# Kernel tuning notes

Measured on AMD Instinct MI355X. Metric: run time of the kernel, lower is better.

## Reference

```python
import jax, jax.numpy as jnp
import numpy as np

D_MODEL = 1024
NUM_HEADS = 16
D_K = D_MODEL // NUM_HEADS
THETA = 10000.0
MAX_SEQ_LEN = 2048
BATCH = 2
SEQ = 2048


def setup_inputs() -> dict:
    key = jax.random.key(0)
    ks = jax.random.split(key, 5)
    std = np.sqrt(2.0 / (D_MODEL + D_MODEL)).astype(np.float32)
    x = jax.random.normal(ks[0], (BATCH, SEQ, D_MODEL), dtype=jnp.float32)
    Wq = jax.random.normal(ks[1], (D_MODEL, D_MODEL), dtype=jnp.float32) * std
    Wk = jax.random.normal(ks[2], (D_MODEL, D_MODEL), dtype=jnp.float32) * std
    Wv = jax.random.normal(ks[3], (D_MODEL, D_MODEL), dtype=jnp.float32) * std
    Wo = jax.random.normal(ks[4], (D_MODEL, D_MODEL), dtype=jnp.float32) * std
    token_positions = jnp.arange(SEQ, dtype=jnp.int32)
    return {"x": x, "token_positions": token_positions,
            "Wq": Wq, "Wk": Wk, "Wv": Wv, "Wo": Wo}


def _rope_tables(positions):
    # freqs: [d_k/2]; angles: [seq, d_k/2]
    freqs = 1.0 / (THETA ** (jnp.arange(0, D_K, 2, dtype=jnp.float32) / D_K))
    angles = positions.astype(jnp.float32)[:, None] * freqs[None, :]
    return jnp.cos(angles), jnp.sin(angles)


def _apply_rope(t, cos, sin):
    # t: [b, h, s, d_k]; cos/sin: [s, d_k/2]; interleaved pair rotation
    x1 = t[..., 0::2]
    x2 = t[..., 1::2]
    r1 = x1 * cos - x2 * sin
    r2 = x1 * sin + x2 * cos
    return jnp.stack([r1, r2], axis=-1).reshape(t.shape)


def reference(x, token_positions, Wq, Wk, Wv, Wo):
    b, s, _ = x.shape
    # projections: y = x W^T
    q = jnp.einsum('bsi,oi->bso', x, Wq)
    k = jnp.einsum('bsi,oi->bso', x, Wk)
    v = jnp.einsum('bsi,oi->bso', x, Wv)
    # split heads: [b, h, s, d]
    q = q.reshape(b, s, NUM_HEADS, D_K).transpose(0, 2, 1, 3)
    k = k.reshape(b, s, NUM_HEADS, D_K).transpose(0, 2, 1, 3)
    v = v.reshape(b, s, NUM_HEADS, D_K).transpose(0, 2, 1, 3)
    cos, sin = _rope_tables(token_positions)
    q = _apply_rope(q, cos, sin)
    k = _apply_rope(k, cos, sin)
    scale = jnp.asarray(D_K, jnp.float32) ** 0.5
    scores = jnp.einsum('bhqd,bhkd->bhqk', q, k) / scale
    causal = jnp.tril(jnp.ones((s, s), dtype=bool))
    scores = jnp.where(causal, scores, -jnp.inf)
    attn = jax.nn.softmax(scores.astype(jnp.float32), axis=-1).astype(scores.dtype)
    out = jnp.einsum('bhqk,bhkd->bhqd', attn, v)
    out = out.transpose(0, 2, 1, 3).reshape(b, s, D_MODEL)
    return jnp.einsum('bsi,oi->bso', out, Wo)
```

## Files before the change

### kernel.cpp

```cpp
#include <hip/hip_runtime.h>
#include <stdint.h>

#define D_MODEL 1024
#define NH      16
#define DKH     64
#define SEQLEN  2048
#define BATCH   2
#define KDIM    1024

typedef __attribute__((ext_vector_type(8))) short          short8;
typedef __attribute__((ext_vector_type(4))) short          bf16x4;
typedef __attribute__((ext_vector_type(8))) unsigned short ushort8;
typedef __attribute__((ext_vector_type(4))) unsigned short usht4;
typedef __attribute__((ext_vector_type(4))) float          f32x4;

#define QSCALE 0.18033688011112042f

__device__ __forceinline__ unsigned short f2bf(float f) {
    union { float f; unsigned u; } v; v.f = f;
    unsigned u = v.u;
    unsigned r = (u + 0x7FFFu + ((u >> 16) & 1u)) >> 16;
    return (unsigned short)r;
}
__device__ __forceinline__ unsigned fbits(float f) {
    union { float f; unsigned u; } v; v.f = f; return v.u;
}

__device__ __forceinline__ void gload_lds16(const unsigned short* g, unsigned short* l) {
    __builtin_amdgcn_global_load_lds(
        (__attribute__((address_space(1))) void*)(g),
        (__attribute__((address_space(3))) void*)(l), 16, 0, 0);
}

__global__ void cvt_all(const float* __restrict__ X,  const float* __restrict__ Wq,
                        const float* __restrict__ Wk, const float* __restrict__ Wv,
                        const float* __restrict__ Wo, const int* __restrict__ pos,
                        unsigned short* __restrict__ Xb,  unsigned short* __restrict__ Wqb,
                        unsigned short* __restrict__ Wkb, unsigned short* __restrict__ Wvb,
                        unsigned short* __restrict__ Wob, float2* __restrict__ tbl) {
    const int z = blockIdx.y;
    if (z == 5) {
        int i = blockIdx.x * 256 + threadIdx.x;
        if (i < 65536) {
            int s = i >> 5, j = i & 31;
            float freq = expf(-((float)(2 * j) * (1.0f / 64.0f)) * 9.210340371976184f);
            float ang = (float)pos[s] * freq;
            float sn, cn;
            sincosf(ang, &sn, &cn);
            tbl[i] = make_float2(cn, sn);
        }
        return;
    }
    const float* src; unsigned short* dst; int n;
    if (z == 0)      { src = X;  dst = Xb;  n = 4194304; }
    else if (z == 1) { src = Wq; dst = Wqb; n = 1048576; }
    else if (z == 2) { src = Wk; dst = Wkb; n = 1048576; }
    else if (z == 3) { src = Wv; dst = Wvb; n = 1048576; }
    else             { src = Wo; dst = Wob; n = 1048576; }
    int i = (blockIdx.x * 256 + threadIdx.x) * 8;
    if (i >= n) return;
    float4 a = *(const float4*)(src + i);
    float4 b = *(const float4*)(src + i + 4);
    ushort8 o;
    o[0] = f2bf(a.x); o[1] = f2bf(a.y); o[2] = f2bf(a.z); o[3] = f2bf(a.w);
    o[4] = f2bf(b.x); o[5] = f2bf(b.y); o[6] = f2bf(b.z); o[7] = f2bf(b.w);
    *(ushort8*)(dst + i) = o;
}

__device__ __forceinline__ void gemm_core_128(
    const unsigned short* __restrict__ A, const unsigned short* __restrict__ W,
    unsigned short* a_lds, unsigned short* b_lds,
    int m0, int n0, f32x4 acc[4][4])
{
    const int tid  = threadIdx.x;
    const int lane = tid & 63;
    const int w    = tid >> 6;
    const int quad = lane >> 4;
    const int l16  = lane & 15;
    const int wm   = w & 1, wn = w >> 1;

    const int srow = lane >> 2;
    const int scol = (lane & 3) * 8;

    #pragma unroll
    for (int mi = 0; mi < 4; mi++)
        #pragma unroll
        for (int ni = 0; ni < 4; ni++) {
            f32x4 z = {0.f, 0.f, 0.f, 0.f};
            acc[mi][ni] = z;
        }

    for (int kk = 0; kk < KDIM; kk += 32) {
        __syncthreads();
        #pragma unroll
        for (int i = 0; i < 2; ++i) {
            int c = 2 * w + i;
            gload_lds16(A + (size_t)(m0 + c * 16 + srow) * KDIM + kk + scol, &a_lds[c * 512]);
            gload_lds16(W + (size_t)(n0 + c * 16 + srow) * KDIM + kk + scol, &b_lds[c * 512]);
        }
        __syncthreads();

        short8 af[4], bf[4];
        #pragma unroll
        for (int i = 0; i < 4; i++) {
            af[i] = *(const short8*)&a_lds[(wm * 64 + i * 16 + l16) * 32 + quad * 8];
            bf[i] = *(const short8*)&b_lds[(wn * 64 + i * 16 + l16) * 32 + quad * 8];
        }
        #pragma unroll
        for (int mi = 0; mi < 4; mi++)
            #pragma unroll
            for (int ni = 0; ni < 4; ni++)
                acc[mi][ni] = __builtin_amdgcn_mfma_f32_16x16x32_bf16(af[mi], bf[ni], acc[mi][ni], 0, 0, 0);
    }
}

__global__ __launch_bounds__(256, 2)
void gemm_qkv(const unsigned short* __restrict__ X,
              const unsigned short* __restrict__ Wq,
              const unsigned short* __restrict__ Wk,
              const unsigned short* __restrict__ Wv,
              const float2* __restrict__ tbl,
              unsigned short* __restrict__ q_ws,
              unsigned short* __restrict__ k_ws,
              unsigned short* __restrict__ v_ws)
{
    __shared__ __align__(16) unsigned short a_lds[128 * 32];
    __shared__ __align__(16) unsigned short b_lds[128 * 32];
    __shared__ __align__(16) unsigned short t_lds[32 * 136];

    const int z = blockIdx.z;
    const unsigned short* W = (z == 0) ? Wq : ((z == 1) ? Wk : Wv);
    const int m0 = blockIdx.x * 128, n0 = blockIdx.y * 128;

    f32x4 acc[4][4];
    gemm_core_128(X, W, a_lds, b_lds, m0, n0, acc);

    const int tid  = threadIdx.x;
    const int lane = tid & 63;
    const int w    = tid >> 6;
    const int quad = lane >> 4;
    const int l16  = lane & 15;
    const int wm   = w & 1, wn = w >> 1;

    if (z == 2) {
        const int bx = m0 >> 11;
        const int c_local_w = wn * 16 + l16;
        const int rd_c = tid >> 3;
        const int rd_s = (tid & 7) * 16;
        #pragma unroll
        for (int ni = 0; ni < 4; ni++) {
            if (ni > 0) __syncthreads();
            #pragma unroll
            for (int mi = 0; mi < 4; mi++) {
                usht4 v4;
                #pragma unroll
                for (int r = 0; r < 4; r++) v4[r] = f2bf(acc[mi][ni][r]);
                *(usht4*)&t_lds[c_local_w * 136 + wm * 64 + mi * 16 + quad * 4] = v4;
            }
            __syncthreads();
            int col = n0 + (rd_c >> 4) * 64 + ni * 16 + (rd_c & 15);
            int h = col >> 6, d = col & 63;
            size_t base = (size_t)(bx * NH + h) * DKH * SEQLEN + (size_t)d * SEQLEN
                        + (m0 & 2047) + rd_s;
            ushort8 x0 = *(ushort8*)&t_lds[rd_c * 136 + rd_s];
            ushort8 x1 = *(ushort8*)&t_lds[rd_c * 136 + rd_s + 8];
            *(ushort8*)&v_ws[base]     = x0;
            *(ushort8*)&v_ws[base + 8] = x1;
        }
    } else {
        unsigned short* dst = (z == 0) ? q_ws : k_ws;
        const float sc = (z == 0) ? QSCALE : 1.0f;
        #pragma unroll
        for (int mi = 0; mi < 4; mi++)
            #pragma unroll
            for (int ni = 0; ni < 4; ni++)
                #pragma unroll
                for (int r = 0; r < 4; r++) {
                    int row = m0 + wm * 64 + mi * 16 + quad * 4 + r;
                    int col = n0 + wn * 64 + ni * 16 + l16;
                    int b = row >> 11, s = row & 2047;
                    int h = col >> 6,  d = col & 63;
                    float val = acc[mi][ni][r];
                    float other = __shfl_xor(val, 1);
                    float2 cs = tbl[s * 32 + (d >> 1)];
                    float rv = (d & 1) ? (other * cs.y + val * cs.x)
                                       : (val * cs.x - other * cs.y);
                    dst[(size_t)(b * NH + h) * SEQLEN * DKH + (size_t)s * DKH + d] =
                        f2bf(rv * sc);
                }
    }
}

__global__ __launch_bounds__(256, 2)
void attn_kernel(const unsigned short* __restrict__ q_ws,
                 const unsigned short* __restrict__ k_ws,
                 const unsigned short* __restrict__ v_ws,
                 unsigned short* __restrict__ ao)
{
    __shared__ __align__(16) unsigned short k_lds[128 * 72];
    __shared__ __align__(16) unsigned short v_lds[64 * 136];

    const int bh  = blockIdx.x;
    const int p   = blockIdx.y;
    const int tid = threadIdx.x, lane = tid & 63, w = tid >> 6;
    const int quad = lane >> 4, l16 = lane & 15;

    const size_t kqbase = (size_t)bh * SEQLEN * DKH;
    const size_t vbase  = (size_t)bh * DKH * SEQLEN;
    const int b = bh >> 4, h = bh & 15;

    const int krow = tid >> 3, kcol = (tid & 7) * 8;
    const int vrow = tid >> 4, vcol = (tid & 15) * 8;

    #pragma unroll
    for (int phase = 0; phase < 2; ++phase) {
        const int qt2 = (phase == 0) ? (15 - p) : p;
        const int q0  = qt2 * 128;
        const int nt  = qt2 + 1;
        const int qwbase = q0 + w * 32;

        short8 aq[2][2];
        #pragma unroll
        for (int st = 0; st < 2; st++)
            #pragma unroll
            for (int kc = 0; kc < 2; kc++)
                aq[st][kc] = *(const short8*)(q_ws + kqbase +
                    (size_t)(qwbase + st * 16 + l16) * DKH + kc * 32 + quad * 8);

        f32x4 o_acc[2][4];
        #pragma unroll
        for (int st = 0; st < 2; st++)
            #pragma unroll
            for (int df = 0; df < 4; df++) { f32x4 z = {0.f,0.f,0.f,0.f}; o_acc[st][df] = z; }
        float lsum[2] = {0.f, 0.f};

        ushort8 kreg[4], vreg[4];
        #pragma unroll
        for (int rr = 0; rr < 4; ++rr) {
            kreg[rr] = *(const ushort8*)(k_ws + kqbase + (size_t)(krow + rr * 32) * DKH + kcol);
            vreg[rr] = *(const ushort8*)(v_ws + vbase + (size_t)(vrow + rr * 16) * SEQLEN + vcol);
        }

        for (int t = 0; t < nt; ++t) {
            const int s0 = t * 128;
            __syncthreads();
            #pragma unroll
            for (int rr = 0; rr < 4; ++rr) {
                *(ushort8*)&k_lds[(krow + rr * 32) * 72 + kcol]  = kreg[rr];
                *(ushort8*)&v_lds[(vrow + rr * 16) * 136 + vcol] = vreg[rr];
            }
            __syncthreads();
            if (t < nt - 1) {
                int s1 = s0 + 128;
                #pragma unroll
                for (int rr = 0; rr < 4; ++rr) {
                    kreg[rr] = *(const ushort8*)(k_ws + kqbase + (size_t)(s1 + krow + rr * 32) * DKH + kcol);
                    vreg[rr] = *(const ushort8*)(v_ws + vbase + (size_t)(vrow + rr * 16) * SEQLEN + s1 + vcol);
                }
            }

            const bool diag = (t == nt - 1);
            #pragma unroll
            for (int nf = 0; nf < 8; nf++) {
                short8 kf0 = *(const short8*)&k_lds[(nf * 16 + l16) * 72 + 0 * 32 + quad * 8];
                short8 kf1 = *(const short8*)&k_lds[(nf * 16 + l16) * 72 + 1 * 32 + quad * 8];
                bf16x4 vf[4];
                #pragma unroll
                for (int df = 0; df < 4; df++)
                    vf[df] = *(const bf16x4*)&v_lds[(df * 16 + l16) * 136 + nf * 16 + quad * 4];

                #pragma unroll
                for (int st = 0; st < 2; st++) {
                    f32x4 s = {0.f,0.f,0.f,0.f};
                    s = __builtin_amdgcn_mfma_f32_16x16x32_bf16(kf0, aq[st][0], s, 0, 0, 0);
                    s = __builtin_amdgcn_mfma_f32_16x16x32_bf16(kf1, aq[st][1], s, 0, 0, 0);

                    if (diag) {
                        int qg = qwbase + st * 16 + l16;
                        int kg = s0 + nf * 16 + quad * 4;
                        #pragma unroll
                        for (int r = 0; r < 4; r++)
                            s[r] = (kg + r <= qg) ? __builtin_amdgcn_exp2f(s[r]) : 0.f;
                    } else {
                        #pragma unroll
                        for (int r = 0; r < 4; r++)
                            s[r] = __builtin_amdgcn_exp2f(s[r]);
                    }
                    lsum[st] += s[0] + s[1] + s[2] + s[3];

                    union { unsigned u[2]; bf16x4 v; } pk;
                    pk.u[0] = __builtin_amdgcn_perm(fbits(s[1]), fbits(s[0]), 0x07060302u);
                    pk.u[1] = __builtin_amdgcn_perm(fbits(s[3]), fbits(s[2]), 0x07060302u);

                    #pragma unroll
                    for (int df = 0; df < 4; df++)
                        o_acc[st][df] = __builtin_amdgcn_mfma_f32_16x16x16bf16_1k(vf[df], pk.v, o_acc[st][df], 0, 0, 0);
                }
            }
        }

        #pragma unroll
        for (int st = 0; st < 2; st++) {
            float rs = lsum[st];
            rs += __shfl_xor(rs, 16);
            rs += __shfl_xor(rs, 32);
            float inv = 1.0f / rs;
            int qg = qwbase + st * 16 + l16;
            #pragma unroll
            for (int df = 0; df < 4; df++) {
                usht4 ov;
                #pragma unroll
                for (int r = 0; r < 4; r++) ov[r] = f2bf(o_acc[st][df][r] * inv);
                *(usht4*)&ao[(size_t)(b * SEQLEN + qg) * D_MODEL + h * DKH + df * 16 + quad * 4] = ov;
            }
        }
    }
}

__global__ __launch_bounds__(256, 2)
void gemm_out(const unsigned short* __restrict__ AO,
              const unsigned short* __restrict__ Wo,
              float* __restrict__ out)
{
    __shared__ __align__(16) unsigned short a_lds[128 * 32];
    __shared__ __align__(16) unsigned short b_lds[128 * 32];

    const int m0 = blockIdx.x * 128, n0 = blockIdx.y * 128;
    f32x4 acc[4][4];
    gemm_core_128(AO, Wo, a_lds, b_lds, m0, n0, acc);

    const int lane = threadIdx.x & 63;
    const int w    = threadIdx.x >> 6;
    const int quad = lane >> 4;
    const int l16  = lane & 15;
    const int wm   = w & 1, wn = w >> 1;

    #pragma unroll
    for (int mi = 0; mi < 4; mi++)
        #pragma unroll
        for (int ni = 0; ni < 4; ni++)
            #pragma unroll
            for (int r = 0; r < 4; r++) {
                int row = m0 + wm * 64 + mi * 16 + quad * 4 + r;
                int col = n0 + wn * 64 + ni * 16 + l16;
                out[(size_t)row * D_MODEL + col] = acc[mi][ni][r];
            }
}

extern "C" void kernel_launch(void* const* d_in, const int* in_sizes, int n_in,
                              void* d_out, int out_size, void* d_ws, size_t ws_size,
                              hipStream_t stream) {
    const float* X  = (const float*)d_in[0];
    const int*   pos = (const int*)d_in[1];
    const float* Wq = (const float*)d_in[2];
    const float* Wk = (const float*)d_in[3];
    const float* Wv = (const float*)d_in[4];
    const float* Wo = (const float*)d_in[5];
    float* out = (float*)d_out;

    unsigned short* Xb  = (unsigned short*)d_ws;
    unsigned short* Wqb = Xb + 4194304;
    unsigned short* Wkb = Wqb + 1048576;
    unsigned short* Wvb = Wkb + 1048576;
    unsigned short* Wob = Wvb + 1048576;
    unsigned short* q_ws = Wob + 1048576;
    unsigned short* k_ws = q_ws + 4194304;
    unsigned short* v_ws = k_ws + 4194304;
    unsigned short* ao   = v_ws + 4194304;
    float2* tbl = (float2*)(ao + 4194304);

    cvt_all<<<dim3(2048, 6), dim3(256), 0, stream>>>(X, Wq, Wk, Wv, Wo, pos,
                                                     Xb, Wqb, Wkb, Wvb, Wob, tbl);
    gemm_qkv<<<dim3(32, 8, 3), dim3(256), 0, stream>>>(Xb, Wqb, Wkb, Wvb, tbl, q_ws, k_ws, v_ws);
    attn_kernel<<<dim3(32, 8), dim3(256), 0, stream>>>(q_ws, k_ws, v_ws, ao);
    gemm_out<<<dim3(32, 8), dim3(256), 0, stream>>>(ao, Wob, out);
}
```

Measured before the change: 176.7 us.

## Split attention KV loop across two blocks and combine partial outputs

The attention kernel gains a third grid dimension that splits each query tile's key/value tiles into two interleaved halves (even and odd tiles), doubling the block count from 256 to 512 for better CU occupancy. Each half writes unnormalized fp32 partial outputs and row sums to workspace, and a new combine kernel adds them, normalizes and converts to bf16. Because the softmax uses a fixed scale with no running max, the partials can simply be added. The cost is an extra launch plus roughly 32MB of fp32 partial traffic written and read back.

```diff
diff --git a/kernel.cpp b/kernel.cpp
--- a/kernel.cpp
+++ b/kernel.cpp
@@ -15,6 +15,7 @@
 typedef __attribute__((ext_vector_type(4))) float          f32x4;
 
 #define QSCALE 0.18033688011112042f
+#define OPART_STRIDE 4194304
 
 __device__ __forceinline__ unsigned short f2bf(float f) {
     union { float f; unsigned u; } v; v.f = f;
@@ -195,19 +196,20 @@
 void attn_kernel(const unsigned short* __restrict__ q_ws,
                  const unsigned short* __restrict__ k_ws,
                  const unsigned short* __restrict__ v_ws,
-                 unsigned short* __restrict__ ao)
+                 float* __restrict__ o_part,
+                 float* __restrict__ l_part)
 {
     __shared__ __align__(16) unsigned short k_lds[128 * 72];
     __shared__ __align__(16) unsigned short v_lds[64 * 136];
 
     const int bh  = blockIdx.x;
     const int p   = blockIdx.y;
+    const int g   = blockIdx.z;
     const int tid = threadIdx.x, lane = tid & 63, w = tid >> 6;
     const int quad = lane >> 4, l16 = lane & 15;
 
     const size_t kqbase = (size_t)bh * SEQLEN * DKH;
     const size_t vbase  = (size_t)bh * DKH * SEQLEN;
-    const int b = bh >> 4, h = bh & 15;
 
     const int krow = tid >> 3, kcol = (tid & 7) * 8;
     const int vrow = tid >> 4, vcol = (tid & 15) * 8;
@@ -235,13 +237,16 @@
         float lsum[2] = {0.f, 0.f};
 
         ushort8 kreg[4], vreg[4];
-        #pragma unroll
-        for (int rr = 0; rr < 4; ++rr) {
-            kreg[rr] = *(const ushort8*)(k_ws + kqbase + (size_t)(krow + rr * 32) * DKH + kcol);
-            vreg[rr] = *(const ushort8*)(v_ws + vbase + (size_t)(vrow + rr * 16) * SEQLEN + vcol);
-        }
-
-        for (int t = 0; t < nt; ++t) {
+        if (g < nt) {
+            int sp = g * 128;
+            #pragma unroll
+            for (int rr = 0; rr < 4; ++rr) {
+                kreg[rr] = *(const ushort8*)(k_ws + kqbase + (size_t)(sp + krow + rr * 32) * DKH + kcol);
+                vreg[rr] = *(const ushort8*)(v_ws + vbase + (size_t)(vrow + rr * 16) * SEQLEN + sp + vcol);
+            }
+        }
+
+        for (int t = g; t < nt; t += 2) {
             const int s0 = t * 128;
             __syncthreads();
             #pragma unroll
@@ -250,8 +255,8 @@
                 *(ushort8*)&v_lds[(vrow + rr * 16) * 136 + vcol] = vreg[rr];
             }
             __syncthreads();
-            if (t < nt - 1) {
-                int s1 = s0 + 128;
+            if (t + 2 < nt) {
+                int s1 = s0 + 256;
                 #pragma unroll
                 for (int rr = 0; rr < 4; ++rr) {
                     kreg[rr] = *(const ushort8*)(k_ws + kqbase + (size_t)(s1 + krow + rr * 32) * DKH + kcol);
@@ -299,22 +304,42 @@
             }
         }
 
+        float* op = o_part + (size_t)g * OPART_STRIDE;
         #pragma unroll
         for (int st = 0; st < 2; st++) {
             float rs = lsum[st];
             rs += __shfl_xor(rs, 16);
             rs += __shfl_xor(rs, 32);
-            float inv = 1.0f / rs;
             int qg = qwbase + st * 16 + l16;
-            #pragma unroll
-            for (int df = 0; df < 4; df++) {
-                usht4 ov;
-                #pragma unroll
-                for (int r = 0; r < 4; r++) ov[r] = f2bf(o_acc[st][df][r] * inv);
-                *(usht4*)&ao[(size_t)(b * SEQLEN + qg) * D_MODEL + h * DKH + df * 16 + quad * 4] = ov;
-            }
+            if (quad == 0)
+                l_part[g * 65536 + bh * SEQLEN + qg] = rs;
+            #pragma unroll
+            for (int df = 0; df < 4; df++)
+                *(f32x4*)&op[((size_t)bh * SEQLEN + qg) * DKH + df * 16 + quad * 4] = o_acc[st][df];
         }
     }
+}
+
+__global__ void combine_kernel(const float* __restrict__ o_part,
+                               const float* __restrict__ l_part,
+                               unsigned short* __restrict__ ao)
+{
+    int i = blockIdx.x * 256 + threadIdx.x;
+    int bh = i >> 14, rem = i & 16383;
+    int q = rem >> 3, c = (rem & 7) * 8;
+    const float* p0 = o_part + ((size_t)bh * SEQLEN + q) * DKH + c;
+    const float* p1 = p0 + OPART_STRIDE;
+    float l = l_part[bh * SEQLEN + q] + l_part[65536 + bh * SEQLEN + q];
+    float inv = 1.0f / l;
+    float4 a0 = *(const float4*)p0, a1 = *(const float4*)(p0 + 4);
+    float4 b0 = *(const float4*)p1, b1 = *(const float4*)(p1 + 4);
+    ushort8 o;
+    o[0] = f2bf((a0.x + b0.x) * inv); o[1] = f2bf((a0.y + b0.y) * inv);
+    o[2] = f2bf((a0.z + b0.z) * inv); o[3] = f2bf((a0.w + b0.w) * inv);
+    o[4] = f2bf((a1.x + b1.x) * inv); o[5] = f2bf((a1.y + b1.y) * inv);
+    o[6] = f2bf((a1.z + b1.z) * inv); o[7] = f2bf((a1.w + b1.w) * inv);
+    int b = bh >> 4, h = bh & 15;
+    *(ushort8*)&ao[(size_t)(b * SEQLEN + q) * D_MODEL + h * DKH + c] = o;
 }
 
 __global__ __launch_bounds__(256, 2)
@@ -367,11 +392,14 @@
     unsigned short* k_ws = q_ws + 4194304;
     unsigned short* v_ws = k_ws + 4194304;
     unsigned short* ao   = v_ws + 4194304;
-    float2* tbl = (float2*)(ao + 4194304);
+    float2* tbl   = (float2*)(ao + 4194304);
+    float* o_part = (float*)(tbl + 65536);
+    float* l_part = o_part + 2 * OPART_STRIDE;
 
     cvt_all<<<dim3(2048, 6), dim3(256), 0, stream>>>(X, Wq, Wk, Wv, Wo, pos,
                                                      Xb, Wqb, Wkb, Wvb, Wob, tbl);
     gemm_qkv<<<dim3(32, 8, 3), dim3(256), 0, stream>>>(Xb, Wqb, Wkb, Wvb, tbl, q_ws, k_ws, v_ws);
-    attn_kernel<<<dim3(32, 8), dim3(256), 0, stream>>>(q_ws, k_ws, v_ws, ao);
+    attn_kernel<<<dim3(32, 8, 2), dim3(256), 0, stream>>>(q_ws, k_ws, v_ws, o_part, l_part);
+    combine_kernel<<<dim3(2048), dim3(256), 0, stream>>>(o_part, l_part, ao);
     gemm_out<<<dim3(32, 8), dim3(256), 0, stream>>>(ao, Wob, out);
 }
```

New measurement: 180.1 us. Within noise of the previous version (+1.9%).
